# Performance work log

Measured on AMD Instinct MI355X. Metric: run time of the kernel, lower is better.

## Reference

```python
import jax, jax.numpy as jnp
import numpy as np

N = 20000      # nodes
E = 320000     # edges (before self-loops)
G = 64         # graphs in batch
H = 4          # attention heads
C = 64         # channels per head
HID = H * C    # 256
IN = 128       # input feature dim
LAT = 64       # latent dim
NEG = 0.2      # LeakyReLU negative slope (PyG GATConv default)
BN_EPS = 1e-5
N_LAYERS = 3


def setup_inputs() -> dict:
    key = jax.random.key(0)
    ks = jax.random.split(key, 24)
    s = 0.1
    return dict(
        x=jax.random.normal(ks[0], (N, IN), jnp.float32),
        edge_index=jax.random.randint(ks[1], (2, E), 0, N, dtype=jnp.int32),
        batch=jnp.sort(jax.random.randint(ks[2], (N,), 0, G, dtype=jnp.int32)),
        W0=jax.random.normal(ks[3], (IN, HID), jnp.float32) * s,
        W_rest=jax.random.normal(ks[4], (N_LAYERS - 1, HID, HID), jnp.float32) * s,
        att_src=jax.random.normal(ks[5], (N_LAYERS, H, C), jnp.float32) * s,
        att_dst=jax.random.normal(ks[6], (N_LAYERS, H, C), jnp.float32) * s,
        bias_conv=jax.random.normal(ks[7], (N_LAYERS, HID), jnp.float32) * s,
        bn_gamma=jax.random.uniform(ks[8], (N_LAYERS, HID), jnp.float32) + 0.5,
        bn_beta=jax.random.normal(ks[9], (N_LAYERS, HID), jnp.float32) * s,
        bn_mean=jax.random.normal(ks[10], (N_LAYERS, HID), jnp.float32) * s,
        bn_var=jax.random.uniform(ks[11], (N_LAYERS, HID), jnp.float32) + 0.5,
        lbn_gamma=jax.random.uniform(ks[12], (HID,), jnp.float32) + 0.5,
        lbn_beta=jax.random.normal(ks[13], (HID,), jnp.float32) * s,
        lbn_mean=jax.random.normal(ks[14], (HID,), jnp.float32) * s,
        lbn_var=jax.random.uniform(ks[15], (HID,), jnp.float32) + 0.5,
        fc_W=jax.random.normal(ks[16], (HID, LAT), jnp.float32) * s,
        fc_b=jax.random.normal(ks[17], (LAT,), jnp.float32) * s,
    )


def _gat_layer(x, src, dst, W, a_src, a_dst, bias):
    # linear transform -> [N, H, C]
    xp = (x @ W).reshape(N, H, C)
    # per-node attention scalars [N, H]
    al_s = (xp * a_src).sum(-1)
    al_d = (xp * a_dst).sum(-1)
    # per-edge logit for edge j->i: leaky_relu(a_s[j] + a_d[i])
    e = jax.nn.leaky_relu(al_s[src] + al_d[dst], NEG)  # [E', H]
    # softmax over incoming edges of each target node
    emax = jax.ops.segment_max(e, dst, num_segments=N)  # [N, H]
    ex = jnp.exp(e - emax[dst])
    denom = jax.ops.segment_sum(ex, dst, num_segments=N)
    alpha = ex / (denom[dst] + 1e-16)
    # weighted scatter-add of source features
    msg = xp[src] * alpha[:, :, None]                    # [E', H, C]
    out = jax.ops.segment_sum(msg, dst, num_segments=N)  # [N, H, C]
    return out.reshape(N, HID) + bias


def _bn_eval(x, gamma, beta, mean, var):
    return (x - mean) * jax.lax.rsqrt(var + BN_EPS) * gamma + beta


def reference(x, edge_index, batch, W0, W_rest, att_src, att_dst, bias_conv,
              bn_gamma, bn_beta, bn_mean, bn_var,
              lbn_gamma, lbn_beta, lbn_mean, lbn_var, fc_W, fc_b):
    # PyG convention: edge_index[0]=source, edge_index[1]=target; GATConv adds self-loops
    loop = jnp.arange(N, dtype=edge_index.dtype)
    src = jnp.concatenate([edge_index[0], loop])
    dst = jnp.concatenate([edge_index[1], loop])
    h = x
    for i in range(N_LAYERS):
        W = W0 if i == 0 else W_rest[i - 1]
        h = _gat_layer(h, src, dst, W, att_src[i], att_dst[i], bias_conv[i])
        h = _bn_eval(h, bn_gamma[i], bn_beta[i], bn_mean[i], bn_var[i])
        h = jax.nn.relu(h)
        # dropout is identity in eval mode
    pooled = jax.ops.segment_sum(h, batch, num_segments=G)  # [G, HID]
    pooled = _bn_eval(pooled, lbn_gamma, lbn_beta, lbn_mean, lbn_var)
    return pooled @ fc_W + fc_b  # [G, LAT]
```

## Files before the change

kernel.cpp:

```cpp
#include <hip/hip_runtime.h>
#include <hip/hip_bf16.h>
#include <cmath>

#define NN   20000
#define NE   320000
#define EE   (NE + NN)
#define NG   64
#define NH   4
#define NC   64
#define HIDD 256
#define IND  128
#define LATD 64
#define NEGS 0.2f
#define BNEPS 1e-5f
#define MPAD 20096
#define PSPLIT 16
#define NB   ((NN + 255) / 256)

#define BM 128
#define BN 64
#define BK 64

typedef __attribute__((ext_vector_type(8))) short short8;
typedef __attribute__((ext_vector_type(4))) float f32x4;

__device__ inline int lower_bound_i(const int* __restrict__ b, int n, int key) {
    int lo = 0, hi = n;
    while (lo < hi) { int mid = (lo + hi) >> 1; if (b[mid] < key) lo = mid + 1; else hi = mid; }
    return lo;
}

__device__ inline float sel4(float4 v, int h) {
    float r = v.x;
    r = (h == 1) ? v.y : r;
    r = (h == 2) ? v.z : r;
    r = (h == 3) ? v.w : r;
    return r;
}

__device__ inline float bf2f(unsigned short u) {
    return __uint_as_float(((unsigned int)u) << 16);
}

__global__ void k_cast_x(const float* __restrict__ x, __hip_bfloat16* __restrict__ hbx) {
    int i = blockIdx.x * blockDim.x + threadIdx.x;
    if (i >= NN * IND / 4) return;
    float4 v = ((const float4*)x)[i];
    union { __hip_bfloat16 b[4]; ushort4 u; } cv;
    cv.b[0] = __float2bfloat16(v.x); cv.b[1] = __float2bfloat16(v.y);
    cv.b[2] = __float2bfloat16(v.z); cv.b[3] = __float2bfloat16(v.w);
    ((ushort4*)hbx)[i] = cv.u;
}

__global__ void k_cast_wt(const float* __restrict__ W, int K, __hip_bfloat16* __restrict__ Wt) {
    int k = blockIdx.x;
    int n = threadIdx.x;
    Wt[(size_t)n * K + k] = __float2bfloat16(W[(size_t)k * HIDD + n]);
}

__global__ void k_hist(const int* __restrict__ ei, int* __restrict__ deg) {
    int e = blockIdx.x * blockDim.x + threadIdx.x;
    if (e >= EE) return;
    int d = (e < NE) ? ei[NE + e] : (e - NE);
    atomicAdd(&deg[d], 1);
}

__global__ __launch_bounds__(256) void k_blocksum(const int* __restrict__ deg,
                                                  int* __restrict__ bsum) {
    __shared__ int s[256];
    int i = blockIdx.x * 256 + threadIdx.x;
    s[threadIdx.x] = (i < NN) ? deg[i] : 0;
    __syncthreads();
    for (int off = 128; off > 0; off >>= 1) {
        if (threadIdx.x < off) s[threadIdx.x] += s[threadIdx.x + off];
        __syncthreads();
    }
    if (threadIdx.x == 0) bsum[blockIdx.x] = s[0];
}

__global__ __launch_bounds__(128) void k_scanbs(const int* __restrict__ bsum,
                                                int* __restrict__ boff,
                                                int* __restrict__ row_ptr) {
    __shared__ int s[128];
    int tid = threadIdx.x;
    int v = (tid < NB) ? bsum[tid] : 0;
    s[tid] = v;
    __syncthreads();
    for (int off = 1; off < 128; off <<= 1) {
        int t = (tid >= off) ? s[tid - off] : 0;
        __syncthreads();
        s[tid] += t;
        __syncthreads();
    }
    if (tid < NB) boff[tid] = s[tid] - v;
    if (tid == NB - 1) row_ptr[NN] = s[tid];
}

__global__ __launch_bounds__(256) void k_scanapply(const int* __restrict__ deg,
                                                   const int* __restrict__ boff,
                                                   int* __restrict__ row_ptr,
                                                   int* __restrict__ cursor) {
    __shared__ int s[256];
    int i = blockIdx.x * 256 + threadIdx.x;
    int v = (i < NN) ? deg[i] : 0;
    s[threadIdx.x] = v;
    __syncthreads();
    for (int off = 1; off < 256; off <<= 1) {
        int t = (threadIdx.x >= off) ? s[threadIdx.x - off] : 0;
        __syncthreads();
        s[threadIdx.x] += t;
        __syncthreads();
    }
    if (i < NN) {
        int excl = boff[blockIdx.x] + s[threadIdx.x] - v;
        row_ptr[i] = excl; cursor[i] = excl;
    }
}

__global__ void k_csr_scatter(const int* __restrict__ ei, int* __restrict__ cursor,
                              int* __restrict__ col_idx) {
    int e = blockIdx.x * blockDim.x + threadIdx.x;
    if (e >= EE) return;
    int s, d;
    if (e < NE) { s = ei[e]; d = ei[NE + e]; } else { s = d = e - NE; }
    int pos = atomicAdd(&cursor[d], 1);
    col_idx[pos] = s;
}

__global__ __launch_bounds__(256) void k_gemm(const short* __restrict__ A,
                                              const short* __restrict__ Bt,
                                              int K, __hip_bfloat16* __restrict__ Cb) {
    __shared__ char As[BM * BK * 2];
    __shared__ char Bs[BN * BK * 2];
    int tid = threadIdx.x;
    int lane = tid & 63;
    int wid = tid >> 6;
    int wm = wid >> 1, wn = wid & 1;
    int bm0 = blockIdx.x * BM, bn0 = blockIdx.y * BN;
    int r16 = lane & 15, kg = lane >> 4;

    f32x4 acc[4][2];
    #pragma unroll
    for (int m = 0; m < 4; ++m)
        #pragma unroll
        for (int n = 0; n < 2; ++n) acc[m][n] = (f32x4){0.f, 0.f, 0.f, 0.f};

    for (int k0 = 0; k0 < K; k0 += BK) {
        __syncthreads();
        #pragma unroll
        for (int p = 0; p < 4; ++p) {
            int row = p * 32 + (tid >> 3);
            int cg  = tid & 7;
            uint4 v = *(const uint4*)(A + (size_t)(bm0 + row) * K + k0 + cg * 8);
            *(uint4*)(As + row * 128 + ((cg * 16) ^ ((row & 7) << 4))) = v;
        }
        #pragma unroll
        for (int p = 0; p < 2; ++p) {
            int row = p * 32 + (tid >> 3);
            int cg  = tid & 7;
            uint4 v = *(const uint4*)(Bt + (size_t)(bn0 + row) * K + k0 + cg * 8);
            *(uint4*)(Bs + row * 128 + ((cg * 16) ^ ((row & 7) << 4))) = v;
        }
        __syncthreads();
        #pragma unroll
        for (int kk = 0; kk < 2; ++kk) {
            short8 af[4], bfr[2];
            int kb = (kk * 32 + kg * 8) * 2;
            #pragma unroll
            for (int m = 0; m < 4; ++m) {
                int row = wm * 64 + m * 16 + r16;
                af[m] = *(const short8*)(As + row * 128 + (kb ^ ((row & 7) << 4)));
            }
            #pragma unroll
            for (int n = 0; n < 2; ++n) {
                int row = wn * 32 + n * 16 + r16;
                bfr[n] = *(const short8*)(Bs + row * 128 + (kb ^ ((row & 7) << 4)));
            }
            #pragma unroll
            for (int m = 0; m < 4; ++m)
                #pragma unroll
                for (int n = 0; n < 2; ++n)
                    acc[m][n] = __builtin_amdgcn_mfma_f32_16x16x32_bf16(af[m], bfr[n], acc[m][n], 0, 0, 0);
        }
    }
    #pragma unroll
    for (int m = 0; m < 4; ++m) {
        int row = bm0 + wm * 64 + m * 16 + kg * 4;
        #pragma unroll
        for (int n = 0; n < 2; ++n) {
            int col = bn0 + wn * 32 + n * 16 + r16;
            #pragma unroll
            for (int r = 0; r < 4; ++r)
                Cb[(size_t)(row + r) * HIDD + col] = __float2bfloat16(acc[m][n][r]);
        }
    }
}

__global__ __launch_bounds__(256) void k_att2(const __hip_bfloat16* __restrict__ xpb,
                                              const float* __restrict__ a_src,
                                              const float* __restrict__ a_dst,
                                              float* __restrict__ al_s,
                                              float* __restrict__ al_d) {
    int wid = threadIdx.x >> 6, lane = threadIdx.x & 63;
    int node = blockIdx.x * 4 + wid;
    if (node >= NN) return;
    int hh = lane >> 4, sub = lane & 15;
    ushort4 u = ((const ushort4*)(xpb + (size_t)node * HIDD))[lane];
    float4 v = {bf2f(u.x), bf2f(u.y), bf2f(u.z), bf2f(u.w)};
    float4 ws = ((const float4*)a_src)[lane];
    float4 wd = ((const float4*)a_dst)[lane];
    float s = v.x * ws.x + v.y * ws.y + v.z * ws.z + v.w * ws.w;
    float d = v.x * wd.x + v.y * wd.y + v.z * wd.z + v.w * wd.w;
    #pragma unroll
    for (int m = 1; m < 16; m <<= 1) {
        s += __shfl_xor(s, m, 64);
        d += __shfl_xor(d, m, 64);
    }
    if (sub == 0) {
        al_s[node * NH + hh] = s;
        al_d[node * NH + hh] = d;
    }
}

__global__ __launch_bounds__(256) void k_gat_agg(
        const int* __restrict__ row_ptr, const int* __restrict__ col_idx,
        const float* __restrict__ al_s, const float* __restrict__ al_d,
        const __hip_bfloat16* __restrict__ xpb,
        const float* __restrict__ bias, const float* __restrict__ bg,
        const float* __restrict__ bb, const float* __restrict__ bm,
        const float* __restrict__ bv,
        float* __restrict__ h, __hip_bfloat16* __restrict__ hb, int wmask) {
    int wid = threadIdx.x >> 6, lane = threadIdx.x & 63;
    int node = blockIdx.x * 4 + wid;
    if (node >= NN) return;
    int lo = row_ptr[node], hi = row_ptr[node + 1];
    int hsel = lane >> 4;
    float adh = sel4(((const float4*)al_d)[node], hsel);

    float4 acc0 = {0,0,0,0}, acc1 = {0,0,0,0}, acc2 = {0,0,0,0}, acc3 = {0,0,0,0};
    float den0 = 0.f, den1 = 0.f, den2 = 0.f, den3 = 0.f;

    int e = lo;
    for (; e + 3 < hi; e += 4) {
        int sc0 = col_idx[e], sc1 = col_idx[e + 1], sc2 = col_idx[e + 2], sc3 = col_idx[e + 3];
        float as0 = al_s[sc0 * NH + hsel];
        float as1 = al_s[sc1 * NH + hsel];
        float as2 = al_s[sc2 * NH + hsel];
        float as3 = al_s[sc3 * NH + hsel];
        ushort4 xv0 = ((const ushort4*)(xpb + (size_t)sc0 * HIDD))[lane];
        ushort4 xv1 = ((const ushort4*)(xpb + (size_t)sc1 * HIDD))[lane];
        ushort4 xv2 = ((const ushort4*)(xpb + (size_t)sc2 * HIDD))[lane];
        ushort4 xv3 = ((const ushort4*)(xpb + (size_t)sc3 * HIDD))[lane];
        float l0 = as0 + adh; l0 = l0 > 0.f ? l0 : NEGS * l0;
        float l1 = as1 + adh; l1 = l1 > 0.f ? l1 : NEGS * l1;
        float l2 = as2 + adh; l2 = l2 > 0.f ? l2 : NEGS * l2;
        float l3 = as3 + adh; l3 = l3 > 0.f ? l3 : NEGS * l3;
        float w0 = __expf(l0), w1 = __expf(l1), w2 = __expf(l2), w3 = __expf(l3);
        den0 += w0; den1 += w1; den2 += w2; den3 += w3;
        acc0.x = fmaf(w0, bf2f(xv0.x), acc0.x); acc0.y = fmaf(w0, bf2f(xv0.y), acc0.y);
        acc0.z = fmaf(w0, bf2f(xv0.z), acc0.z); acc0.w = fmaf(w0, bf2f(xv0.w), acc0.w);
        acc1.x = fmaf(w1, bf2f(xv1.x), acc1.x); acc1.y = fmaf(w1, bf2f(xv1.y), acc1.y);
        acc1.z = fmaf(w1, bf2f(xv1.z), acc1.z); acc1.w = fmaf(w1, bf2f(xv1.w), acc1.w);
        acc2.x = fmaf(w2, bf2f(xv2.x), acc2.x); acc2.y = fmaf(w2, bf2f(xv2.y), acc2.y);
        acc2.z = fmaf(w2, bf2f(xv2.z), acc2.z); acc2.w = fmaf(w2, bf2f(xv2.w), acc2.w);
        acc3.x = fmaf(w3, bf2f(xv3.x), acc3.x); acc3.y = fmaf(w3, bf2f(xv3.y), acc3.y);
        acc3.z = fmaf(w3, bf2f(xv3.z), acc3.z); acc3.w = fmaf(w3, bf2f(xv3.w), acc3.w);
    }
    for (; e < hi; ++e) {
        int sc = col_idx[e];
        float as = al_s[sc * NH + hsel];
        ushort4 xv = ((const ushort4*)(xpb + (size_t)sc * HIDD))[lane];
        float l = as + adh; l = l > 0.f ? l : NEGS * l;
        float wt = __expf(l);
        den0 += wt;
        acc0.x = fmaf(wt, bf2f(xv.x), acc0.x); acc0.y = fmaf(wt, bf2f(xv.y), acc0.y);
        acc0.z = fmaf(wt, bf2f(xv.z), acc0.z); acc0.w = fmaf(wt, bf2f(xv.w), acc0.w);
    }

    float inv = 1.f / ((den0 + den1) + (den2 + den3) + 1e-16f);
    float4 acc;
    acc.x = ((acc0.x + acc1.x) + (acc2.x + acc3.x)) * inv;
    acc.y = ((acc0.y + acc1.y) + (acc2.y + acc3.y)) * inv;
    acc.z = ((acc0.z + acc1.z) + (acc2.z + acc3.z)) * inv;
    acc.w = ((acc0.w + acc1.w) + (acc2.w + acc3.w)) * inv;

    float4 bi = ((const float4*)bias)[lane];
    float4 gg = ((const float4*)bg)[lane];
    float4 be = ((const float4*)bb)[lane];
    float4 mn = ((const float4*)bm)[lane];
    float4 vr = ((const float4*)bv)[lane];
    float4 val;
    val.x = (acc.x + bi.x - mn.x) * rsqrtf(vr.x + BNEPS) * gg.x + be.x;
    val.y = (acc.y + bi.y - mn.y) * rsqrtf(vr.y + BNEPS) * gg.y + be.y;
    val.z = (acc.z + bi.z - mn.z) * rsqrtf(vr.z + BNEPS) * gg.z + be.z;
    val.w = (acc.w + bi.w - mn.w) * rsqrtf(vr.w + BNEPS) * gg.w + be.w;
    val.x = val.x > 0.f ? val.x : 0.f;
    val.y = val.y > 0.f ? val.y : 0.f;
    val.z = val.z > 0.f ? val.z : 0.f;
    val.w = val.w > 0.f ? val.w : 0.f;
    if (wmask & 1)
        ((float4*)h)[(size_t)node * 64 + lane] = val;
    if (wmask & 2) {
        union { __hip_bfloat16 b[4]; ushort4 u; } cv;
        cv.b[0] = __float2bfloat16(val.x); cv.b[1] = __float2bfloat16(val.y);
        cv.b[2] = __float2bfloat16(val.z); cv.b[3] = __float2bfloat16(val.w);
        ((ushort4*)hb)[(size_t)node * 64 + lane] = cv.u;
    }
}

__global__ void k_pool2(const float* __restrict__ h, const int* __restrict__ batch,
                        float* __restrict__ partial) {
    int g = blockIdx.x, i = blockIdx.y, col = threadIdx.x;
    int lo = lower_bound_i(batch, NN, g);
    int hi = lower_bound_i(batch, NN, g + 1);
    int len = hi - lo;
    int a = lo + (int)((long)len * i / PSPLIT);
    int b = lo + (int)((long)len * (i + 1) / PSPLIT);
    float acc = 0.f;
    for (int n = a; n < b; ++n) acc += h[(size_t)n * HIDD + col];
    partial[((size_t)g * PSPLIT + i) * HIDD + col] = acc;
}

__global__ __launch_bounds__(64) void k_final(const float* __restrict__ partial,
                                              const float* __restrict__ lg,
                                              const float* __restrict__ lb,
                                              const float* __restrict__ lm,
                                              const float* __restrict__ lv,
                                              const float* __restrict__ fcW,
                                              const float* __restrict__ fcb,
                                              float* __restrict__ out) {
    __shared__ float ps[HIDD];
    int g = blockIdx.x, j = threadIdx.x;
    for (int k = j; k < HIDD; k += 64) {
        float s = 0.f;
        for (int i = 0; i < PSPLIT; ++i)
            s += partial[((size_t)g * PSPLIT + i) * HIDD + k];
        ps[k] = (s - lm[k]) * rsqrtf(lv[k] + BNEPS) * lg[k] + lb[k];
    }
    __syncthreads();
    float acc = 0.f;
    for (int k = 0; k < HIDD; ++k)
        acc = fmaf(ps[k], fcW[k * LATD + j], acc);
    out[g * LATD + j] = acc + fcb[j];
}

extern "C" void kernel_launch(void* const* d_in, const int* in_sizes, int n_in,
                              void* d_out, int out_size, void* d_ws, size_t ws_size,
                              hipStream_t stream) {
    const float* x     = (const float*)d_in[0];
    const int*   ei    = (const int*)d_in[1];
    const int*   batch = (const int*)d_in[2];
    const float* W0    = (const float*)d_in[3];
    const float* Wr    = (const float*)d_in[4];
    const float* asrc  = (const float*)d_in[5];
    const float* adst  = (const float*)d_in[6];
    const float* bconv = (const float*)d_in[7];
    const float* bng   = (const float*)d_in[8];
    const float* bnb   = (const float*)d_in[9];
    const float* bnm   = (const float*)d_in[10];
    const float* bnv   = (const float*)d_in[11];
    const float* lg    = (const float*)d_in[12];
    const float* lb    = (const float*)d_in[13];
    const float* lm    = (const float*)d_in[14];
    const float* lv    = (const float*)d_in[15];
    const float* fcW   = (const float*)d_in[16];
    const float* fcb   = (const float*)d_in[17];
    float* out = (float*)d_out;

    char* w = (char*)d_ws;
    size_t off = 0;
    auto alloc = [&](size_t bytes) {
        char* p = w + off;
        off += (bytes + 255) / 256 * 256;
        return p;
    };
    float* hbuf  = (float*)alloc((size_t)NN * HIDD * 4);
    float* al_s  = (float*)alloc((size_t)NN * NH * 4);
    float* al_d  = (float*)alloc((size_t)NN * NH * 4);
    float* partial = (float*)alloc((size_t)NG * PSPLIT * HIDD * 4);
    __hip_bfloat16* hbx = (__hip_bfloat16*)alloc((size_t)MPAD * IND * 2);
    __hip_bfloat16* hb2 = (__hip_bfloat16*)alloc((size_t)MPAD * HIDD * 2);
    __hip_bfloat16* xpb = (__hip_bfloat16*)alloc((size_t)MPAD * HIDD * 2);
    __hip_bfloat16* Wt  = (__hip_bfloat16*)alloc((size_t)HIDD * HIDD * 2);
    int* deg     = (int*)alloc((size_t)NN * 4);
    int* row_ptr = (int*)alloc((size_t)(NN + 1) * 4);
    int* cursor  = (int*)alloc((size_t)NN * 4);
    int* col_idx = (int*)alloc((size_t)EE * 4);
    int* bsum    = (int*)alloc((size_t)NB * 4);
    int* boff    = (int*)alloc((size_t)NB * 4);

    hipMemsetAsync(deg, 0, (size_t)NN * sizeof(int), stream);
    hipLaunchKernelGGL(k_hist, dim3((EE + 255) / 256), dim3(256), 0, stream, ei, deg);
    hipLaunchKernelGGL(k_blocksum, dim3(NB), dim3(256), 0, stream, deg, bsum);
    hipLaunchKernelGGL(k_scanbs, dim3(1), dim3(128), 0, stream, bsum, boff, row_ptr);
    hipLaunchKernelGGL(k_scanapply, dim3(NB), dim3(256), 0, stream, deg, boff, row_ptr, cursor);
    hipLaunchKernelGGL(k_csr_scatter, dim3((EE + 255) / 256), dim3(256), 0, stream,
                       ei, cursor, col_idx);

    hipLaunchKernelGGL(k_cast_x, dim3((NN * IND / 4 + 255) / 256), dim3(256), 0, stream, x, hbx);

    for (int layer = 0; layer < 3; ++layer) {
        const float* W = (layer == 0) ? W0 : (Wr + (size_t)(layer - 1) * HIDD * HIDD);
        int K          = (layer == 0) ? IND : HIDD;
        const __hip_bfloat16* Ab = (layer == 0) ? hbx : hb2;
        int wmask      = (layer == 2) ? 1 : 2;

        hipLaunchKernelGGL(k_cast_wt, dim3(K), dim3(HIDD), 0, stream, W, K, Wt);
        hipLaunchKernelGGL(k_gemm, dim3(MPAD / BM, HIDD / BN), dim3(256), 0, stream,
                           (const short*)Ab, (const short*)Wt, K, xpb);
        hipLaunchKernelGGL(k_att2, dim3((NN + 3) / 4), dim3(256), 0, stream,
                           xpb, asrc + layer * NH * NC, adst + layer * NH * NC, al_s, al_d);
        hipLaunchKernelGGL(k_gat_agg, dim3((NN + 3) / 4), dim3(256), 0, stream,
                           row_ptr, col_idx, al_s, al_d, xpb,
                           bconv + layer * HIDD, bng + layer * HIDD, bnb + layer * HIDD,
                           bnm + layer * HIDD, bnv + layer * HIDD, hbuf, hb2, wmask);
    }

    hipLaunchKernelGGL(k_pool2, dim3(NG, PSPLIT), dim3(HIDD), 0, stream, hbuf, batch, partial);
    hipLaunchKernelGGL(k_final, dim3(NG), dim3(LATD), 0, stream,
                       partial, lg, lb, lm, lv, fcW, fcb, out);
}
```

Before: 205.6 us.

## Split each node's edge aggregation across four wavefronts with LDS reduction

```diff
diff --git a/kernel.cpp b/kernel.cpp
--- a/kernel.cpp
+++ b/kernel.cpp
@@ -40,6 +40,11 @@
 
 __device__ inline float bf2f(unsigned short u) {
     return __uint_as_float(((unsigned int)u) << 16);
+}
+
+__global__ void k_zero(int* __restrict__ p, int n) {
+    int i = blockIdx.x * blockDim.x + threadIdx.x;
+    if (i < n) p[i] = 0;
 }
 
 __global__ void k_cast_x(const float* __restrict__ x, __hip_bfloat16* __restrict__ hbx) {
@@ -230,43 +235,34 @@
         const float* __restrict__ bb, const float* __restrict__ bm,
         const float* __restrict__ bv,
         float* __restrict__ h, __hip_bfloat16* __restrict__ hb, int wmask) {
-    int wid = threadIdx.x >> 6, lane = threadIdx.x & 63;
-    int node = blockIdx.x * 4 + wid;
-    if (node >= NN) return;
+    __shared__ float lacc[4][HIDD];
+    __shared__ float lden[4][NH];
+    int node = blockIdx.x;
+    int wv = threadIdx.x >> 6, lane = threadIdx.x & 63;
     int lo = row_ptr[node], hi = row_ptr[node + 1];
     int hsel = lane >> 4;
     float adh = sel4(((const float4*)al_d)[node], hsel);
 
-    float4 acc0 = {0,0,0,0}, acc1 = {0,0,0,0}, acc2 = {0,0,0,0}, acc3 = {0,0,0,0};
-    float den0 = 0.f, den1 = 0.f, den2 = 0.f, den3 = 0.f;
-
-    int e = lo;
-    for (; e + 3 < hi; e += 4) {
-        int sc0 = col_idx[e], sc1 = col_idx[e + 1], sc2 = col_idx[e + 2], sc3 = col_idx[e + 3];
+    float4 acc0 = {0,0,0,0}, acc1 = {0,0,0,0};
+    float den0 = 0.f, den1 = 0.f;
+
+    int e = lo + wv;
+    for (; e + 4 < hi; e += 8) {
+        int sc0 = col_idx[e], sc1 = col_idx[e + 4];
         float as0 = al_s[sc0 * NH + hsel];
         float as1 = al_s[sc1 * NH + hsel];
-        float as2 = al_s[sc2 * NH + hsel];
-        float as3 = al_s[sc3 * NH + hsel];
         ushort4 xv0 = ((const ushort4*)(xpb + (size_t)sc0 * HIDD))[lane];
         ushort4 xv1 = ((const ushort4*)(xpb + (size_t)sc1 * HIDD))[lane];
-        ushort4 xv2 = ((const ushort4*)(xpb + (size_t)sc2 * HIDD))[lane];
-        ushort4 xv3 = ((const ushort4*)(xpb + (size_t)sc3 * HIDD))[lane];
         float l0 = as0 + adh; l0 = l0 > 0.f ? l0 : NEGS * l0;
         float l1 = as1 + adh; l1 = l1 > 0.f ? l1 : NEGS * l1;
-        float l2 = as2 + adh; l2 = l2 > 0.f ? l2 : NEGS * l2;
-        float l3 = as3 + adh; l3 = l3 > 0.f ? l3 : NEGS * l3;
-        float w0 = __expf(l0), w1 = __expf(l1), w2 = __expf(l2), w3 = __expf(l3);
-        den0 += w0; den1 += w1; den2 += w2; den3 += w3;
+        float w0 = __expf(l0), w1 = __expf(l1);
+        den0 += w0; den1 += w1;
         acc0.x = fmaf(w0, bf2f(xv0.x), acc0.x); acc0.y = fmaf(w0, bf2f(xv0.y), acc0.y);
         acc0.z = fmaf(w0, bf2f(xv0.z), acc0.z); acc0.w = fmaf(w0, bf2f(xv0.w), acc0.w);
         acc1.x = fmaf(w1, bf2f(xv1.x), acc1.x); acc1.y = fmaf(w1, bf2f(xv1.y), acc1.y);
         acc1.z = fmaf(w1, bf2f(xv1.z), acc1.z); acc1.w = fmaf(w1, bf2f(xv1.w), acc1.w);
-        acc2.x = fmaf(w2, bf2f(xv2.x), acc2.x); acc2.y = fmaf(w2, bf2f(xv2.y), acc2.y);
-        acc2.z = fmaf(w2, bf2f(xv2.z), acc2.z); acc2.w = fmaf(w2, bf2f(xv2.w), acc2.w);
-        acc3.x = fmaf(w3, bf2f(xv3.x), acc3.x); acc3.y = fmaf(w3, bf2f(xv3.y), acc3.y);
-        acc3.z = fmaf(w3, bf2f(xv3.z), acc3.z); acc3.w = fmaf(w3, bf2f(xv3.w), acc3.w);
-    }
-    for (; e < hi; ++e) {
+    }
+    if (e < hi) {
         int sc = col_idx[e];
         float as = al_s[sc * NH + hsel];
         ushort4 xv = ((const ushort4*)(xpb + (size_t)sc * HIDD))[lane];
@@ -277,12 +273,23 @@
         acc0.z = fmaf(wt, bf2f(xv.z), acc0.z); acc0.w = fmaf(wt, bf2f(xv.w), acc0.w);
     }
 
-    float inv = 1.f / ((den0 + den1) + (den2 + den3) + 1e-16f);
+    float4 pa = {acc0.x + acc1.x, acc0.y + acc1.y, acc0.z + acc1.z, acc0.w + acc1.w};
+    ((float4*)lacc[wv])[lane] = pa;
+    if ((lane & 15) == 0) lden[wv][hsel] = den0 + den1;
+    __syncthreads();
+    if (wv != 0) return;
+
+    float4 a0 = ((const float4*)lacc[0])[lane];
+    float4 a1 = ((const float4*)lacc[1])[lane];
+    float4 a2 = ((const float4*)lacc[2])[lane];
+    float4 a3 = ((const float4*)lacc[3])[lane];
+    float den = (lden[0][hsel] + lden[1][hsel]) + (lden[2][hsel] + lden[3][hsel]);
+    float inv = 1.f / (den + 1e-16f);
     float4 acc;
-    acc.x = ((acc0.x + acc1.x) + (acc2.x + acc3.x)) * inv;
-    acc.y = ((acc0.y + acc1.y) + (acc2.y + acc3.y)) * inv;
-    acc.z = ((acc0.z + acc1.z) + (acc2.z + acc3.z)) * inv;
-    acc.w = ((acc0.w + acc1.w) + (acc2.w + acc3.w)) * inv;
+    acc.x = ((a0.x + a1.x) + (a2.x + a3.x)) * inv;
+    acc.y = ((a0.y + a1.y) + (a2.y + a3.y)) * inv;
+    acc.z = ((a0.z + a1.z) + (a2.z + a3.z)) * inv;
+    acc.w = ((a0.w + a1.w) + (a2.w + a3.w)) * inv;
 
     float4 bi = ((const float4*)bias)[lane];
     float4 gg = ((const float4*)bg)[lane];
@@ -389,7 +396,7 @@
     int* bsum    = (int*)alloc((size_t)NB * 4);
     int* boff    = (int*)alloc((size_t)NB * 4);
 
-    hipMemsetAsync(deg, 0, (size_t)NN * sizeof(int), stream);
+    hipLaunchKernelGGL(k_zero, dim3(NB), dim3(256), 0, stream, deg, NN);
     hipLaunchKernelGGL(k_hist, dim3((EE + 255) / 256), dim3(256), 0, stream, ei, deg);
     hipLaunchKernelGGL(k_blocksum, dim3(NB), dim3(256), 0, stream, deg, bsum);
     hipLaunchKernelGGL(k_scanbs, dim3(1), dim3(128), 0, stream, bsum, boff, row_ptr);
@@ -410,7 +417,7 @@
                            (const short*)Ab, (const short*)Wt, K, xpb);
         hipLaunchKernelGGL(k_att2, dim3((NN + 3) / 4), dim3(256), 0, stream,
                            xpb, asrc + layer * NH * NC, adst + layer * NH * NC, al_s, al_d);
-        hipLaunchKernelGGL(k_gat_agg, dim3((NN + 3) / 4), dim3(256), 0, stream,
+        hipLaunchKernelGGL(k_gat_agg, dim3(NN), dim3(256), 0, stream,
                            row_ptr, col_idx, al_s, al_d, xpb,
                            bconv + layer * HIDD, bng + layer * HIDD, bnb + layer * HIDD,
                            bnm + layer * HIDD, bnv + layer * HIDD, hbuf, hb2, wmask);
```

Measured after the change: 225.6 us. 9.8% more time.

## Precompute per-edge attention weights in a separate kernel before aggregation

Applied to the files above, without the earlier changes.

```diff
diff --git a/kernel.cpp b/kernel.cpp
--- a/kernel.cpp
+++ b/kernel.cpp
@@ -30,16 +30,13 @@
     return lo;
 }
 
-__device__ inline float sel4(float4 v, int h) {
-    float r = v.x;
-    r = (h == 1) ? v.y : r;
-    r = (h == 2) ? v.z : r;
-    r = (h == 3) ? v.w : r;
-    return r;
-}
-
 __device__ inline float bf2f(unsigned short u) {
     return __uint_as_float(((unsigned int)u) << 16);
+}
+
+__global__ void k_zero(int* __restrict__ p, int n) {
+    int i = blockIdx.x * blockDim.x + threadIdx.x;
+    if (i < n) p[i] = 0;
 }
 
 __global__ void k_cast_x(const float* __restrict__ x, __hip_bfloat16* __restrict__ hbx) {
@@ -52,10 +49,16 @@
     ((ushort4*)hbx)[i] = cv.u;
 }
 
-__global__ void k_cast_wt(const float* __restrict__ W, int K, __hip_bfloat16* __restrict__ Wt) {
+__global__ void k_cast_wt_all(const float* __restrict__ W0, const float* __restrict__ Wr,
+                              __hip_bfloat16* __restrict__ Wt3) {
     int k = blockIdx.x;
+    int l = blockIdx.y;
     int n = threadIdx.x;
-    Wt[(size_t)n * K + k] = __float2bfloat16(W[(size_t)k * HIDD + n]);
+    int K = (l == 0) ? IND : HIDD;
+    if (k >= K) return;
+    const float* W = (l == 0) ? W0 : (Wr + (size_t)(l - 1) * HIDD * HIDD);
+    size_t off = (l == 0) ? 0 : ((size_t)HIDD * IND + (size_t)(l - 1) * HIDD * HIDD);
+    Wt3[off + (size_t)n * K + k] = __float2bfloat16(W[(size_t)k * HIDD + n]);
 }
 
 __global__ void k_hist(const int* __restrict__ ei, int* __restrict__ deg) {
@@ -118,13 +121,14 @@
 }
 
 __global__ void k_csr_scatter(const int* __restrict__ ei, int* __restrict__ cursor,
-                              int* __restrict__ col_idx) {
+                              int* __restrict__ col_idx, int* __restrict__ dst_srt) {
     int e = blockIdx.x * blockDim.x + threadIdx.x;
     if (e >= EE) return;
     int s, d;
     if (e < NE) { s = ei[e]; d = ei[NE + e]; } else { s = d = e - NE; }
     int pos = atomicAdd(&cursor[d], 1);
     col_idx[pos] = s;
+    dst_srt[pos] = d;
 }
 
 __global__ __launch_bounds__(256) void k_gemm(const short* __restrict__ A,
@@ -222,9 +226,33 @@
     }
 }
 
+__global__ void k_edgew(const int* __restrict__ col_idx, const int* __restrict__ dst_srt,
+                        const float* __restrict__ al_s, const float* __restrict__ al_d,
+                        float* __restrict__ ew) {
+    int e = blockIdx.x * blockDim.x + threadIdx.x;
+    if (e >= EE) return;
+    int s = col_idx[e], d = dst_srt[e];
+    float4 as = ((const float4*)al_s)[s];
+    float4 ad = ((const float4*)al_d)[d];
+    float4 l;
+    l.x = as.x + ad.x; l.x = l.x > 0.f ? l.x : NEGS * l.x;
+    l.y = as.y + ad.y; l.y = l.y > 0.f ? l.y : NEGS * l.y;
+    l.z = as.z + ad.z; l.z = l.z > 0.f ? l.z : NEGS * l.z;
+    l.w = as.w + ad.w; l.w = l.w > 0.f ? l.w : NEGS * l.w;
+    float4 w = {__expf(l.x), __expf(l.y), __expf(l.z), __expf(l.w)};
+    ((float4*)ew)[e] = w;
+}
+
+#define EDGE_BODY(I) \
+    { den##I += w##I; \
+      acc##I.x = fmaf(w##I, bf2f(xv##I.x), acc##I.x); \
+      acc##I.y = fmaf(w##I, bf2f(xv##I.y), acc##I.y); \
+      acc##I.z = fmaf(w##I, bf2f(xv##I.z), acc##I.z); \
+      acc##I.w = fmaf(w##I, bf2f(xv##I.w), acc##I.w); }
+
 __global__ __launch_bounds__(256) void k_gat_agg(
         const int* __restrict__ row_ptr, const int* __restrict__ col_idx,
-        const float* __restrict__ al_s, const float* __restrict__ al_d,
+        const float* __restrict__ ew,
         const __hip_bfloat16* __restrict__ xpb,
         const float* __restrict__ bias, const float* __restrict__ bg,
         const float* __restrict__ bb, const float* __restrict__ bm,
@@ -235,7 +263,6 @@
     if (node >= NN) return;
     int lo = row_ptr[node], hi = row_ptr[node + 1];
     int hsel = lane >> 4;
-    float adh = sel4(((const float4*)al_d)[node], hsel);
 
     float4 acc0 = {0,0,0,0}, acc1 = {0,0,0,0}, acc2 = {0,0,0,0}, acc3 = {0,0,0,0};
     float den0 = 0.f, den1 = 0.f, den2 = 0.f, den3 = 0.f;
@@ -243,41 +270,25 @@
     int e = lo;
     for (; e + 3 < hi; e += 4) {
         int sc0 = col_idx[e], sc1 = col_idx[e + 1], sc2 = col_idx[e + 2], sc3 = col_idx[e + 3];
-        float as0 = al_s[sc0 * NH + hsel];
-        float as1 = al_s[sc1 * NH + hsel];
-        float as2 = al_s[sc2 * NH + hsel];
-        float as3 = al_s[sc3 * NH + hsel];
+        float w0 = ew[(size_t)e * NH + hsel];
+        float w1 = ew[(size_t)(e + 1) * NH + hsel];
+        float w2 = ew[(size_t)(e + 2) * NH + hsel];
+        float w3 = ew[(size_t)(e + 3) * NH + hsel];
         ushort4 xv0 = ((const ushort4*)(xpb + (size_t)sc0 * HIDD))[lane];
         ushort4 xv1 = ((const ushort4*)(xpb + (size_t)sc1 * HIDD))[lane];
         ushort4 xv2 = ((const ushort4*)(xpb + (size_t)sc2 * HIDD))[lane];
         ushort4 xv3 = ((const ushort4*)(xpb + (size_t)sc3 * HIDD))[lane];
-        float l0 = as0 + adh; l0 = l0 > 0.f ? l0 : NEGS * l0;
-        float l1 = as1 + adh; l1 = l1 > 0.f ? l1 : NEGS * l1;
-        float l2 = as2 + adh; l2 = l2 > 0.f ? l2 : NEGS * l2;
-        float l3 = as3 + adh; l3 = l3 > 0.f ? l3 : NEGS * l3;
-        float w0 = __expf(l0), w1 = __expf(l1), w2 = __expf(l2), w3 = __expf(l3);
-        den0 += w0; den1 += w1; den2 += w2; den3 += w3;
-        acc0.x = fmaf(w0, bf2f(xv0.x), acc0.x); acc0.y = fmaf(w0, bf2f(xv0.y), acc0.y);
-        acc0.z = fmaf(w0, bf2f(xv0.z), acc0.z); acc0.w = fmaf(w0, bf2f(xv0.w), acc0.w);
-        acc1.x = fmaf(w1, bf2f(xv1.x), acc1.x); acc1.y = fmaf(w1, bf2f(xv1.y), acc1.y);
-        acc1.z = fmaf(w1, bf2f(xv1.z), acc1.z); acc1.w = fmaf(w1, bf2f(xv1.w), acc1.w);
-        acc2.x = fmaf(w2, bf2f(xv2.x), acc2.x); acc2.y = fmaf(w2, bf2f(xv2.y), acc2.y);
-        acc2.z = fmaf(w2, bf2f(xv2.z), acc2.z); acc2.w = fmaf(w2, bf2f(xv2.w), acc2.w);
-        acc3.x = fmaf(w3, bf2f(xv3.x), acc3.x); acc3.y = fmaf(w3, bf2f(xv3.y), acc3.y);
-        acc3.z = fmaf(w3, bf2f(xv3.z), acc3.z); acc3.w = fmaf(w3, bf2f(xv3.w), acc3.w);
+        EDGE_BODY(0) EDGE_BODY(1) EDGE_BODY(2) EDGE_BODY(3)
     }
     for (; e < hi; ++e) {
-        int sc = col_idx[e];
-        float as = al_s[sc * NH + hsel];
-        ushort4 xv = ((const ushort4*)(xpb + (size_t)sc * HIDD))[lane];
-        float l = as + adh; l = l > 0.f ? l : NEGS * l;
-        float wt = __expf(l);
-        den0 += wt;
-        acc0.x = fmaf(wt, bf2f(xv.x), acc0.x); acc0.y = fmaf(wt, bf2f(xv.y), acc0.y);
-        acc0.z = fmaf(wt, bf2f(xv.z), acc0.z); acc0.w = fmaf(wt, bf2f(xv.w), acc0.w);
-    }
-
-    float inv = 1.f / ((den0 + den1) + (den2 + den3) + 1e-16f);
+        int sc0 = col_idx[e];
+        float w0 = ew[(size_t)e * NH + hsel];
+        ushort4 xv0 = ((const ushort4*)(xpb + (size_t)sc0 * HIDD))[lane];
+        EDGE_BODY(0)
+    }
+
+    float den = (den0 + den1) + (den2 + den3);
+    float inv = 1.f / (den + 1e-16f);
     float4 acc;
     acc.x = ((acc0.x + acc1.x) + (acc2.x + acc3.x)) * inv;
     acc.y = ((acc0.y + acc1.y) + (acc2.y + acc3.y)) * inv;
@@ -377,41 +388,46 @@
     float* hbuf  = (float*)alloc((size_t)NN * HIDD * 4);
     float* al_s  = (float*)alloc((size_t)NN * NH * 4);
     float* al_d  = (float*)alloc((size_t)NN * NH * 4);
+    float* ewbuf = (float*)alloc((size_t)EE * NH * 4);
     float* partial = (float*)alloc((size_t)NG * PSPLIT * HIDD * 4);
     __hip_bfloat16* hbx = (__hip_bfloat16*)alloc((size_t)MPAD * IND * 2);
     __hip_bfloat16* hb2 = (__hip_bfloat16*)alloc((size_t)MPAD * HIDD * 2);
     __hip_bfloat16* xpb = (__hip_bfloat16*)alloc((size_t)MPAD * HIDD * 2);
-    __hip_bfloat16* Wt  = (__hip_bfloat16*)alloc((size_t)HIDD * HIDD * 2);
+    __hip_bfloat16* Wt3 = (__hip_bfloat16*)alloc(((size_t)HIDD * IND + 2 * (size_t)HIDD * HIDD) * 2);
     int* deg     = (int*)alloc((size_t)NN * 4);
     int* row_ptr = (int*)alloc((size_t)(NN + 1) * 4);
     int* cursor  = (int*)alloc((size_t)NN * 4);
     int* col_idx = (int*)alloc((size_t)EE * 4);
+    int* dst_srt = (int*)alloc((size_t)EE * 4);
     int* bsum    = (int*)alloc((size_t)NB * 4);
     int* boff    = (int*)alloc((size_t)NB * 4);
 
-    hipMemsetAsync(deg, 0, (size_t)NN * sizeof(int), stream);
+    hipLaunchKernelGGL(k_zero, dim3(NB), dim3(256), 0, stream, deg, NN);
     hipLaunchKernelGGL(k_hist, dim3((EE + 255) / 256), dim3(256), 0, stream, ei, deg);
     hipLaunchKernelGGL(k_blocksum, dim3(NB), dim3(256), 0, stream, deg, bsum);
     hipLaunchKernelGGL(k_scanbs, dim3(1), dim3(128), 0, stream, bsum, boff, row_ptr);
     hipLaunchKernelGGL(k_scanapply, dim3(NB), dim3(256), 0, stream, deg, boff, row_ptr, cursor);
     hipLaunchKernelGGL(k_csr_scatter, dim3((EE + 255) / 256), dim3(256), 0, stream,
-                       ei, cursor, col_idx);
+                       ei, cursor, col_idx, dst_srt);
 
     hipLaunchKernelGGL(k_cast_x, dim3((NN * IND / 4 + 255) / 256), dim3(256), 0, stream, x, hbx);
+    hipLaunchKernelGGL(k_cast_wt_all, dim3(HIDD, 3), dim3(HIDD), 0, stream, W0, Wr, Wt3);
+
+    const size_t wtoff[3] = {0, (size_t)HIDD * IND, (size_t)HIDD * IND + (size_t)HIDD * HIDD};
 
     for (int layer = 0; layer < 3; ++layer) {
-        const float* W = (layer == 0) ? W0 : (Wr + (size_t)(layer - 1) * HIDD * HIDD);
-        int K          = (layer == 0) ? IND : HIDD;
+        int K = (layer == 0) ? IND : HIDD;
         const __hip_bfloat16* Ab = (layer == 0) ? hbx : hb2;
-        int wmask      = (layer == 2) ? 1 : 2;
-
-        hipLaunchKernelGGL(k_cast_wt, dim3(K), dim3(HIDD), 0, stream, W, K, Wt);
+        int wmask = (layer == 2) ? 1 : 2;
+
         hipLaunchKernelGGL(k_gemm, dim3(MPAD / BM, HIDD / BN), dim3(256), 0, stream,
-                           (const short*)Ab, (const short*)Wt, K, xpb);
+                           (const short*)Ab, (const short*)(Wt3 + wtoff[layer]), K, xpb);
         hipLaunchKernelGGL(k_att2, dim3((NN + 3) / 4), dim3(256), 0, stream,
                            xpb, asrc + layer * NH * NC, adst + layer * NH * NC, al_s, al_d);
+        hipLaunchKernelGGL(k_edgew, dim3((EE + 255) / 256), dim3(256), 0, stream,
+                           col_idx, dst_srt, al_s, al_d, ewbuf);
         hipLaunchKernelGGL(k_gat_agg, dim3((NN + 3) / 4), dim3(256), 0, stream,
-                           row_ptr, col_idx, al_s, al_d, xpb,
+                           row_ptr, col_idx, ewbuf, xpb,
                            bconv + layer * HIDD, bng + layer * HIDD, bnb + layer * HIDD,
                            bnm + layer * HIDD, bnv + layer * HIDD, hbuf, hb2, wmask);
     }
```

Result: slower. 214.0 us (+4.1%).
